# Kernel tuning notes

Hardware: AMD Instinct MI355X
Metric: run time of the kernel (lower is better)

## Reference

```python
import jax, jax.numpy as jnp
import numpy as np

EPS = 1e-12  # F.normalize default eps

def _l2_normalize(x, axis):
    # matches torch F.normalize: x / max(||x||_2, eps)
    n = jnp.sqrt(jnp.sum(x * x, axis=axis, keepdims=True))
    return x / jnp.maximum(n, EPS)

def setup_inputs() -> dict:
    key = jax.random.key(0)
    k1, k2 = jax.random.split(key)
    N, B, C = 4096, 16, 512
    x_pre = jax.random.normal(k1, (N, B, C), dtype=jnp.float32)
    x_pos = jax.random.normal(k2, (N, B, C), dtype=jnp.float32)
    return {"x_pre": x_pre, "x_pos": x_pos}

def reference(x_pre, x_pos):
    # [N, B, C]
    fea_pred = _l2_normalize(x_pre, axis=2)
    fea_later = _l2_normalize(x_pos, axis=2)
    # Original does a full bmm [B, N, N] then takes the diagonal; the diagonal
    # is just the per-token dot product (cosine similarity). Same math.
    dis = jnp.sum(fea_pred * fea_later, axis=2, keepdims=True)  # [N, B, 1]
    weight = 1.0 - jax.nn.sigmoid(dis)
    return x_pos * weight
```

## Files before the change

kernel.cpp:

```cpp
#include <hip/hip_runtime.h>


constexpr int C_DIM = 512;
constexpr int ROWS  = 4096 * 16;

__global__ __launch_bounds__(256) void tokenmixer_kernel(
    const float* __restrict__ pre,
    const float* __restrict__ pos,
    float* __restrict__ out)
{
    const int row  = (int)((blockIdx.x * 256u + threadIdx.x) >> 6);
    const int lane = (int)(threadIdx.x & 63u);
    const size_t base = (size_t)row * C_DIM + (size_t)lane * 8;

    const float4 p0 = *reinterpret_cast<const float4*>(pre + base);
    const float4 p1 = *reinterpret_cast<const float4*>(pre + base + 4);
    const float4 q0 = *reinterpret_cast<const float4*>(pos + base);
    const float4 q1 = *reinterpret_cast<const float4*>(pos + base + 4);

    float pf[8] = {p0.x, p0.y, p0.z, p0.w, p1.x, p1.y, p1.z, p1.w};
    float qf[8] = {q0.x, q0.y, q0.z, q0.w, q1.x, q1.y, q1.z, q1.w};

    float s_pre = 0.f, s_pos = 0.f, dot = 0.f;
#pragma unroll
    for (int i = 0; i < 8; ++i) {
        s_pre = fmaf(pf[i], pf[i], s_pre);
        s_pos = fmaf(qf[i], qf[i], s_pos);
        dot   = fmaf(pf[i], qf[i], dot);
    }

#pragma unroll
    for (int m = 1; m < 64; m <<= 1) {
        s_pre += __shfl_xor(s_pre, m, 64);
        s_pos += __shfl_xor(s_pos, m, 64);
        dot   += __shfl_xor(dot,   m, 64);
    }

    const float n_pre = fmaxf(sqrtf(s_pre), 1e-12f);
    const float n_pos = fmaxf(sqrtf(s_pos), 1e-12f);
    const float cosv  = dot / (n_pre * n_pos);
    const float w = 1.0f / (1.0f + __expf(cosv));

    float4 o0, o1;
    o0.x = qf[0] * w; o0.y = qf[1] * w; o0.z = qf[2] * w; o0.w = qf[3] * w;
    o1.x = qf[4] * w; o1.y = qf[5] * w; o1.z = qf[6] * w; o1.w = qf[7] * w;
    *reinterpret_cast<float4*>(out + base)     = o0;
    *reinterpret_cast<float4*>(out + base + 4) = o1;
}

extern "C" void kernel_launch(void* const* d_in, const int* in_sizes, int n_in,
                              void* d_out, int out_size, void* d_ws, size_t ws_size,
                              hipStream_t stream) {
    const float* pre = (const float*)d_in[0];
    const float* pos = (const float*)d_in[1];
    float* out = (float*)d_out;

    const int blocks = ROWS / 4;
    tokenmixer_kernel<<<blocks, 256, 0, stream>>>(pre, pos, out);
}
```

Baseline: 300.8 us.

## Use persistent grid-stride waves with register prefetch and nontemporal stores

Switches from one row per wave across 16384 blocks to a fixed grid of 2048 blocks, where each wave loops over 8 rows and prefetches the next row's inputs into registers while computing the current one. The lane layout changes so each lane loads two float4s 256 floats apart, keeping each wave's loads fully coalesced. Output uses nontemporal stores to avoid polluting cache. The extra loop iteration at the end issues a redundant reload of the first row, and the smaller grid may reduce the memory parallelism available.

```diff
diff --git a/kernel.cpp b/kernel.cpp
--- a/kernel.cpp
+++ b/kernel.cpp
@@ -1,51 +1,72 @@
 #include <hip/hip_runtime.h>
 
 
-constexpr int C_DIM = 512;
-constexpr int ROWS  = 4096 * 16;
+typedef float f32x4 __attribute__((ext_vector_type(4)));
 
-__global__ __launch_bounds__(256) void tokenmixer_kernel(
+constexpr int C_DIM  = 512;
+constexpr int ROWS   = 4096 * 16;
+constexpr int BLOCKS = 2048;
+constexpr int WAVES  = BLOCKS * 4;
+constexpr int ITERS  = ROWS / WAVES;
+
+__global__ __launch_bounds__(256, 8) void tokenmixer_kernel(
     const float* __restrict__ pre,
     const float* __restrict__ pos,
     float* __restrict__ out)
 {
-    const int row  = (int)((blockIdx.x * 256u + threadIdx.x) >> 6);
+    const int wave = (int)((blockIdx.x * 256u + threadIdx.x) >> 6);
     const int lane = (int)(threadIdx.x & 63u);
-    const size_t base = (size_t)row * C_DIM + (size_t)lane * 8;
+    const size_t lo = (size_t)(lane * 4);
 
-    const float4 p0 = *reinterpret_cast<const float4*>(pre + base);
-    const float4 p1 = *reinterpret_cast<const float4*>(pre + base + 4);
-    const float4 q0 = *reinterpret_cast<const float4*>(pos + base);
-    const float4 q1 = *reinterpret_cast<const float4*>(pos + base + 4);
+    int row = wave;
+    size_t base = (size_t)row * C_DIM + lo;
 
-    float pf[8] = {p0.x, p0.y, p0.z, p0.w, p1.x, p1.y, p1.z, p1.w};
-    float qf[8] = {q0.x, q0.y, q0.z, q0.w, q1.x, q1.y, q1.z, q1.w};
+    f32x4 pA = *(const f32x4*)(pre + base);
+    f32x4 pB = *(const f32x4*)(pre + base + 256);
+    f32x4 qA = *(const f32x4*)(pos + base);
+    f32x4 qB = *(const f32x4*)(pos + base + 256);
 
-    float s_pre = 0.f, s_pos = 0.f, dot = 0.f;
-#pragma unroll
-    for (int i = 0; i < 8; ++i) {
-        s_pre = fmaf(pf[i], pf[i], s_pre);
-        s_pos = fmaf(qf[i], qf[i], s_pos);
-        dot   = fmaf(pf[i], qf[i], dot);
+    #pragma unroll 1
+    for (int it = 0; it < ITERS; ++it) {
+        const int nrow = (it + 1 < ITERS) ? (row + WAVES) : wave;
+        const size_t nb = (size_t)nrow * C_DIM + lo;
+        f32x4 npA = *(const f32x4*)(pre + nb);
+        f32x4 npB = *(const f32x4*)(pre + nb + 256);
+        f32x4 nqA = *(const f32x4*)(pos + nb);
+        f32x4 nqB = *(const f32x4*)(pos + nb + 256);
+
+        float s_pre = 0.f, s_pos = 0.f, dot = 0.f;
+        #pragma unroll
+        for (int i = 0; i < 4; ++i) {
+            s_pre = fmaf(pA[i], pA[i], s_pre);
+            s_pre = fmaf(pB[i], pB[i], s_pre);
+            s_pos = fmaf(qA[i], qA[i], s_pos);
+            s_pos = fmaf(qB[i], qB[i], s_pos);
+            dot   = fmaf(pA[i], qA[i], dot);
+            dot   = fmaf(pB[i], qB[i], dot);
+        }
+
+        #pragma unroll
+        for (int m = 1; m < 64; m <<= 1) {
+            s_pre += __shfl_xor(s_pre, m, 64);
+            s_pos += __shfl_xor(s_pos, m, 64);
+            dot   += __shfl_xor(dot,   m, 64);
+        }
+
+        const float n_pre = fmaxf(sqrtf(s_pre), 1e-12f);
+        const float n_pos = fmaxf(sqrtf(s_pos), 1e-12f);
+        const float cosv  = dot / (n_pre * n_pos);
+        const float w = 1.0f / (1.0f + __expf(cosv));
+
+        const f32x4 oA = qA * w;
+        const f32x4 oB = qB * w;
+        __builtin_nontemporal_store(oA, (f32x4*)(out + base));
+        __builtin_nontemporal_store(oB, (f32x4*)(out + base + 256));
+
+        row  = nrow;
+        base = nb;
+        pA = npA; pB = npB; qA = nqA; qB = nqB;
     }
-
-#pragma unroll
-    for (int m = 1; m < 64; m <<= 1) {
-        s_pre += __shfl_xor(s_pre, m, 64);
-        s_pos += __shfl_xor(s_pos, m, 64);
-        dot   += __shfl_xor(dot,   m, 64);
-    }
-
-    const float n_pre = fmaxf(sqrtf(s_pre), 1e-12f);
-    const float n_pos = fmaxf(sqrtf(s_pos), 1e-12f);
-    const float cosv  = dot / (n_pre * n_pos);
-    const float w = 1.0f / (1.0f + __expf(cosv));
-
-    float4 o0, o1;
-    o0.x = qf[0] * w; o0.y = qf[1] * w; o0.z = qf[2] * w; o0.w = qf[3] * w;
-    o1.x = qf[4] * w; o1.y = qf[5] * w; o1.z = qf[6] * w; o1.w = qf[7] * w;
-    *reinterpret_cast<float4*>(out + base)     = o0;
-    *reinterpret_cast<float4*>(out + base + 4) = o1;
 }
 
 extern "C" void kernel_launch(void* const* d_in, const int* in_sizes, int n_in,
@@ -55,6 +76,5 @@
     const float* pos = (const float*)d_in[1];
     float* out = (float*)d_out;
 
-    const int blocks = ROWS / 4;
-    tokenmixer_kernel<<<blocks, 256, 0, stream>>>(pre, pos, out);
+    tokenmixer_kernel<<<BLOCKS, 256, 0, stream>>>(pre, pos, out);
 }
```

Measured after the change: 320.0 us. 1.06x slower.

## Process four rows per wave with software-pipelined loads and sched barriers

Applied to the files above, without the earlier changes.

Each wave now handles four rows instead of one, and the grid shrinks by four. Loads for later rows are issued ahead of the computation on earlier rows, with sched_barrier fences keeping that order. Each row is read as two strided 16-byte chunks, and the launch bounds ask for 6 waves per SIMD. The aim is more memory-level parallelism per wave on this bandwidth-bound kernel, at the cost of more registers and fewer waves overall.

```diff
diff --git a/kernel.cpp b/kernel.cpp
--- a/kernel.cpp
+++ b/kernel.cpp
@@ -1,51 +1,78 @@
 #include <hip/hip_runtime.h>
 
+
+typedef float f32x4 __attribute__((ext_vector_type(4)));
 
 constexpr int C_DIM = 512;
 constexpr int ROWS  = 4096 * 16;
 
-__global__ __launch_bounds__(256) void tokenmixer_kernel(
+__device__ __forceinline__ f32x4 ld4(const float* p) {
+    return *reinterpret_cast<const f32x4*>(p);
+}
+
+__global__ __launch_bounds__(256, 6) void tokenmixer_kernel(
     const float* __restrict__ pre,
     const float* __restrict__ pos,
     float* __restrict__ out)
 {
-    const int row  = (int)((blockIdx.x * 256u + threadIdx.x) >> 6);
+    const int wave = (int)((blockIdx.x * 256u + threadIdx.x) >> 6);
     const int lane = (int)(threadIdx.x & 63u);
-    const size_t base = (size_t)row * C_DIM + (size_t)lane * 8;
 
-    const float4 p0 = *reinterpret_cast<const float4*>(pre + base);
-    const float4 p1 = *reinterpret_cast<const float4*>(pre + base + 4);
-    const float4 q0 = *reinterpret_cast<const float4*>(pos + base);
-    const float4 q1 = *reinterpret_cast<const float4*>(pos + base + 4);
+    const size_t base = (size_t)(4 * wave) * C_DIM + (size_t)(lane * 4);
+    const float* pp = pre + base;
+    const float* qq = pos + base;
+    float*       oo = out + base;
 
-    float pf[8] = {p0.x, p0.y, p0.z, p0.w, p1.x, p1.y, p1.z, p1.w};
-    float qf[8] = {q0.x, q0.y, q0.z, q0.w, q1.x, q1.y, q1.z, q1.w};
+    f32x4 pA0,pB0,pA1,pB1,pA2,pB2,pA3,pB3;
+    f32x4 qA0,qB0,qA1,qB1,qA2,qB2,qA3,qB3;
 
-    float s_pre = 0.f, s_pos = 0.f, dot = 0.f;
-#pragma unroll
-    for (int i = 0; i < 8; ++i) {
-        s_pre = fmaf(pf[i], pf[i], s_pre);
-        s_pos = fmaf(qf[i], qf[i], s_pos);
-        dot   = fmaf(pf[i], qf[i], dot);
-    }
+    pA0 = ld4(pp);        pB0 = ld4(pp + 256);
+    pA1 = ld4(pp + 512);  pB1 = ld4(pp + 768);
+    qA0 = ld4(qq);        qB0 = ld4(qq + 256);
+    __builtin_amdgcn_sched_barrier(0);
 
-#pragma unroll
-    for (int m = 1; m < 64; m <<= 1) {
-        s_pre += __shfl_xor(s_pre, m, 64);
-        s_pos += __shfl_xor(s_pos, m, 64);
-        dot   += __shfl_xor(dot,   m, 64);
-    }
+    pA2 = ld4(pp + 1024); pB2 = ld4(pp + 1280);
+    qA1 = ld4(qq + 512);  qB1 = ld4(qq + 768);
+    __builtin_amdgcn_sched_barrier(0);
 
-    const float n_pre = fmaxf(sqrtf(s_pre), 1e-12f);
-    const float n_pos = fmaxf(sqrtf(s_pos), 1e-12f);
-    const float cosv  = dot / (n_pre * n_pos);
-    const float w = 1.0f / (1.0f + __expf(cosv));
+    auto compute = [&](f32x4 pA, f32x4 pB, f32x4 qA, f32x4 qB, float* dst) {
+        float sp = 0.f, sq = 0.f, d = 0.f;
+        #pragma unroll
+        for (int i = 0; i < 4; ++i) {
+            sp = fmaf(pA[i], pA[i], sp); sp = fmaf(pB[i], pB[i], sp);
+            sq = fmaf(qA[i], qA[i], sq); sq = fmaf(qB[i], qB[i], sq);
+            d  = fmaf(pA[i], qA[i], d);  d  = fmaf(pB[i], qB[i], d);
+        }
+        #pragma unroll
+        for (int m = 1; m < 64; m <<= 1) {
+            sp += __shfl_xor(sp, m, 64);
+            sq += __shfl_xor(sq, m, 64);
+            d  += __shfl_xor(d,  m, 64);
+        }
+        const float np = fmaxf(sqrtf(sp), 1e-12f);
+        const float nq = fmaxf(sqrtf(sq), 1e-12f);
+        const float w  = 1.0f / (1.0f + __expf(d / (np * nq)));
+        *reinterpret_cast<f32x4*>(dst)       = qA * w;
+        *reinterpret_cast<f32x4*>(dst + 256) = qB * w;
+    };
 
-    float4 o0, o1;
-    o0.x = qf[0] * w; o0.y = qf[1] * w; o0.z = qf[2] * w; o0.w = qf[3] * w;
-    o1.x = qf[4] * w; o1.y = qf[5] * w; o1.z = qf[6] * w; o1.w = qf[7] * w;
-    *reinterpret_cast<float4*>(out + base)     = o0;
-    *reinterpret_cast<float4*>(out + base + 4) = o1;
+    compute(pA0, pB0, qA0, qB0, oo);
+    __builtin_amdgcn_sched_barrier(0);
+
+    pA3 = ld4(pp + 1536); pB3 = ld4(pp + 1792);
+    qA2 = ld4(qq + 1024); qB2 = ld4(qq + 1280);
+    __builtin_amdgcn_sched_barrier(0);
+
+    compute(pA1, pB1, qA1, qB1, oo + 512);
+    __builtin_amdgcn_sched_barrier(0);
+
+    qA3 = ld4(qq + 1536); qB3 = ld4(qq + 1792);
+    __builtin_amdgcn_sched_barrier(0);
+
+    compute(pA2, pB2, qA2, qB2, oo + 1024);
+    __builtin_amdgcn_sched_barrier(0);
+
+    compute(pA3, pB3, qA3, qB3, oo + 1536);
 }
 
 extern "C" void kernel_launch(void* const* d_in, const int* in_sizes, int n_in,
@@ -55,6 +82,6 @@
     const float* pos = (const float*)d_in[1];
     float* out = (float*)d_out;
 
-    const int blocks = ROWS / 4;
+    const int blocks = ROWS / 16;
     tokenmixer_kernel<<<blocks, 256, 0, stream>>>(pre, pos, out);
 }
```

After: 310.9 us. 1.03x slower.

## Split fused kernel into weight computation and scaling passes via workspace

Applied to the files above, without the earlier changes.

When enough workspace is available, the single fused kernel becomes two kernels. The first reads both inputs and writes one weight per row; the second rereads pos and writes the scaled output. This adds a full second read of pos, which is 128MB of extra traffic, on top of an extra launch. The intent is presumably that the second pass gets L2/MALL cache hits or better overlap, but the kernel is memory-bound and the extra traffic is likely to hurt.

```diff
diff --git a/kernel.cpp b/kernel.cpp
--- a/kernel.cpp
+++ b/kernel.cpp
@@ -1,51 +1,95 @@
 #include <hip/hip_runtime.h>
 
+
+typedef float f32x4 __attribute__((ext_vector_type(4)));
 
 constexpr int C_DIM = 512;
 constexpr int ROWS  = 4096 * 16;
 
-__global__ __launch_bounds__(256) void tokenmixer_kernel(
+__global__ __launch_bounds__(256) void weights_kernel(
+    const float* __restrict__ pre,
+    const float* __restrict__ pos,
+    float* __restrict__ w)
+{
+    const int row  = (int)((blockIdx.x * 256u + threadIdx.x) >> 6);
+    const int lane = (int)(threadIdx.x & 63u);
+    const size_t base = (size_t)row * C_DIM + (size_t)(lane * 8);
+
+    const f32x4 p0 = *(const f32x4*)(pre + base);
+    const f32x4 p1 = *(const f32x4*)(pre + base + 4);
+    const f32x4 q0 = *(const f32x4*)(pos + base);
+    const f32x4 q1 = *(const f32x4*)(pos + base + 4);
+
+    float sp = 0.f, sq = 0.f, d = 0.f;
+#pragma unroll
+    for (int i = 0; i < 4; ++i) {
+        sp = fmaf(p0[i], p0[i], sp); sp = fmaf(p1[i], p1[i], sp);
+        sq = fmaf(q0[i], q0[i], sq); sq = fmaf(q1[i], q1[i], sq);
+        d  = fmaf(p0[i], q0[i], d);  d  = fmaf(p1[i], q1[i], d);
+    }
+#pragma unroll
+    for (int m = 1; m < 64; m <<= 1) {
+        sp += __shfl_xor(sp, m, 64);
+        sq += __shfl_xor(sq, m, 64);
+        d  += __shfl_xor(d,  m, 64);
+    }
+    if (lane == 0) {
+        const float np = fmaxf(sqrtf(sp), 1e-12f);
+        const float nq = fmaxf(sqrtf(sq), 1e-12f);
+        w[row] = 1.0f / (1.0f + __expf(d / (np * nq)));
+    }
+}
+
+__global__ __launch_bounds__(256) void scale_kernel(
+    const float* __restrict__ pos,
+    const float* __restrict__ w,
+    float* __restrict__ out)
+{
+    const int row  = (int)((blockIdx.x * 256u + threadIdx.x) >> 6);
+    const int lane = (int)(threadIdx.x & 63u);
+    const size_t base = (size_t)row * C_DIM + (size_t)(lane * 8);
+
+    const f32x4 q0 = *(const f32x4*)(pos + base);
+    const f32x4 q1 = *(const f32x4*)(pos + base + 4);
+    const float wv = w[row];
+
+    *(f32x4*)(out + base)     = q0 * wv;
+    *(f32x4*)(out + base + 4) = q1 * wv;
+}
+
+__global__ __launch_bounds__(256) void fused_kernel(
     const float* __restrict__ pre,
     const float* __restrict__ pos,
     float* __restrict__ out)
 {
     const int row  = (int)((blockIdx.x * 256u + threadIdx.x) >> 6);
     const int lane = (int)(threadIdx.x & 63u);
-    const size_t base = (size_t)row * C_DIM + (size_t)lane * 8;
+    const size_t base = (size_t)row * C_DIM + (size_t)(lane * 8);
 
-    const float4 p0 = *reinterpret_cast<const float4*>(pre + base);
-    const float4 p1 = *reinterpret_cast<const float4*>(pre + base + 4);
-    const float4 q0 = *reinterpret_cast<const float4*>(pos + base);
-    const float4 q1 = *reinterpret_cast<const float4*>(pos + base + 4);
+    const f32x4 p0 = *(const f32x4*)(pre + base);
+    const f32x4 p1 = *(const f32x4*)(pre + base + 4);
+    const f32x4 q0 = *(const f32x4*)(pos + base);
+    const f32x4 q1 = *(const f32x4*)(pos + base + 4);
 
-    float pf[8] = {p0.x, p0.y, p0.z, p0.w, p1.x, p1.y, p1.z, p1.w};
-    float qf[8] = {q0.x, q0.y, q0.z, q0.w, q1.x, q1.y, q1.z, q1.w};
-
-    float s_pre = 0.f, s_pos = 0.f, dot = 0.f;
+    float sp = 0.f, sq = 0.f, d = 0.f;
 #pragma unroll
-    for (int i = 0; i < 8; ++i) {
-        s_pre = fmaf(pf[i], pf[i], s_pre);
-        s_pos = fmaf(qf[i], qf[i], s_pos);
-        dot   = fmaf(pf[i], qf[i], dot);
+    for (int i = 0; i < 4; ++i) {
+        sp = fmaf(p0[i], p0[i], sp); sp = fmaf(p1[i], p1[i], sp);
+        sq = fmaf(q0[i], q0[i], sq); sq = fmaf(q1[i], q1[i], sq);
+        d  = fmaf(p0[i], q0[i], d);  d  = fmaf(p1[i], q1[i], d);
     }
-
 #pragma unroll
     for (int m = 1; m < 64; m <<= 1) {
-        s_pre += __shfl_xor(s_pre, m, 64);
-        s_pos += __shfl_xor(s_pos, m, 64);
-        dot   += __shfl_xor(dot,   m, 64);
+        sp += __shfl_xor(sp, m, 64);
+        sq += __shfl_xor(sq, m, 64);
+        d  += __shfl_xor(d,  m, 64);
     }
+    const float np = fmaxf(sqrtf(sp), 1e-12f);
+    const float nq = fmaxf(sqrtf(sq), 1e-12f);
+    const float wv = 1.0f / (1.0f + __expf(d / (np * nq)));
 
-    const float n_pre = fmaxf(sqrtf(s_pre), 1e-12f);
-    const float n_pos = fmaxf(sqrtf(s_pos), 1e-12f);
-    const float cosv  = dot / (n_pre * n_pos);
-    const float w = 1.0f / (1.0f + __expf(cosv));
-
-    float4 o0, o1;
-    o0.x = qf[0] * w; o0.y = qf[1] * w; o0.z = qf[2] * w; o0.w = qf[3] * w;
-    o1.x = qf[4] * w; o1.y = qf[5] * w; o1.z = qf[6] * w; o1.w = qf[7] * w;
-    *reinterpret_cast<float4*>(out + base)     = o0;
-    *reinterpret_cast<float4*>(out + base + 4) = o1;
+    *(f32x4*)(out + base)     = q0 * wv;
+    *(f32x4*)(out + base + 4) = q1 * wv;
 }
 
 extern "C" void kernel_launch(void* const* d_in, const int* in_sizes, int n_in,
@@ -56,5 +100,12 @@
     float* out = (float*)d_out;
 
     const int blocks = ROWS / 4;
-    tokenmixer_kernel<<<blocks, 256, 0, stream>>>(pre, pos, out);
+
+    if (ws_size >= (size_t)ROWS * sizeof(float)) {
+        float* w = (float*)d_ws;
+        weights_kernel<<<blocks, 256, 0, stream>>>(pre, pos, w);
+        scale_kernel<<<blocks, 256, 0, stream>>>(pos, w, out);
+    } else {
+        fused_kernel<<<blocks, 256, 0, stream>>>(pre, pos, out);
+    }
 }
```

Measured after the change: 334.6 us. +11.2%, slower.
